# Kernel optimization log

Measured on AMD Instinct MI355X. Metric: run time of the kernel, lower is better.

The kernel has to match this reference:

```python
import jax, jax.numpy as jnp
import numpy as np

D = 256; H = 8; DH = D // H; FF = 1024; L = 2048; M = 1024


def _mlp(x, w0, b0, w1, b1, w2, b2):
    # 3-layer MLP, relu on all but last (matches MLP class)
    x = jax.nn.relu(x @ w0 + b0)
    x = jax.nn.relu(x @ w1 + b1)
    return x @ w2 + b2


def _ln(x, g, b, eps=1e-5):
    m = jnp.mean(x, axis=-1, keepdims=True)
    v = jnp.var(x, axis=-1, keepdims=True)
    return (x - m) * jax.lax.rsqrt(v + eps) * g + b


def setup_inputs():
    key = jax.random.key(0)
    ks = jax.random.split(key, 16)
    p = lambda i, shape: jax.random.normal(ks[i], shape, jnp.float32) * 0.02
    z = lambda *s: jnp.zeros(s, jnp.float32)
    o = lambda *s: jnp.ones(s, jnp.float32)
    # positions: ego covers [0, L), agent covers [L-M, 2L-M) -> exactly M shared positions
    return {
        'ego_q': jax.random.normal(ks[0], (1, L, D), jnp.float32),
        'agent_q': jax.random.normal(ks[1], (1, L, D), jnp.float32),
        'ego_pos': jnp.arange(L, dtype=jnp.int32),
        'agent_pos': jnp.arange(L, dtype=jnp.int32) + (L - M),
        'n_match': M,
        'fw0': p(2, (2 * D, D)), 'fb0': z(D),
        'fw1': p(3, (D, D)), 'fb1': z(D),
        'fw2': p(4, (D, D)), 'fb2': z(D),
        'wq': p(5, (D, D)), 'bq': z(D),
        'wk': p(6, (D, D)), 'bk': z(D),
        'wv': p(7, (D, D)), 'bv': z(D),
        'wo': p(8, (D, D)), 'bo': z(D),
        'g1': o(D), 'be1': z(D),
        'l1w': p(9, (D, FF)), 'l1b': z(FF),
        'l2w': p(10, (FF, D)), 'l2b': z(D),
        'g2': o(D), 'be2': z(D),
    }


def reference(ego_q, agent_q, ego_pos, agent_pos, n_match,
              fw0, fb0, fw1, fb1, fw2, fb2,
              wq, bq, wk, bk, wv, bv, wo, bo,
              g1, be1, l1w, l1b, l2w, l2b, g2, be2):
    La = agent_pos.shape[0]
    # vectorized replacement of the per-position dict/loop grouping:
    # for each ego position, find a matching agent position (positions sorted+unique)
    idx = jnp.clip(jnp.searchsorted(agent_pos, ego_pos), 0, La - 1)
    matched = (agent_pos[idx] == ego_pos)                     # (L,)
    pair = jnp.concatenate([ego_q, agent_q[:, idx, :]], axis=-1)  # (1, L, 2D)
    fused = _mlp(pair, fw0, fb0, fw1, fb1, fw2, fb2)          # (1, L, D)
    ego_out = jnp.where(matched[None, :, None], fused, ego_q)
    # agent queries whose positions are NOT in ego's set: indices [n_match, La)
    q = jnp.concatenate([ego_out, agent_q[:, n_match:, :]], axis=1)  # (1, 2L-M, D)
    kv = jnp.concatenate([ego_q, agent_q], axis=1)                   # (1, 2L, D)
    # MultiheadAttention (batch_first, eval mode -> no dropout)
    qh = (q @ wq + bq).reshape(1, -1, H, DH)
    kh = (kv @ wk + bk).reshape(1, -1, H, DH)
    vh = (kv @ wv + bv).reshape(1, -1, H, DH)
    scores = jnp.einsum('bqhd,bkhd->bhqk', qh, kh) * (1.0 / np.sqrt(DH))
    attn = jax.nn.softmax(scores, axis=-1)
    o = jnp.einsum('bhqk,bkhd->bqhd', attn, vh).reshape(1, -1, D) @ wo + bo
    x = _ln(q + o, g1, be1)
    ff = jax.nn.relu(x @ l1w + l1b) @ l2w + l2b
    return _ln(x + ff, g2, be2)
```

## Files before the change

kernel.cpp:

```cpp
#include <hip/hip_runtime.h>
#include <hip/hip_bf16.h>

typedef __hip_bfloat16 bf16;
typedef __bf16 bf16x8 __attribute__((ext_vector_type(8)));
typedef float  f32x16 __attribute__((ext_vector_type(16)));

__device__ __forceinline__ bool is_bf16_flag(const unsigned* g1w) {
    return *g1w == 0x3F803F80u;
}

__device__ __forceinline__ unsigned cvt_pk_bf16(float lo, float hi) {
    unsigned w;
    asm("v_cvt_pk_bf16_f32 %0, %1, %2" : "=v"(w) : "v"(lo), "v"(hi));
    return w;
}
__device__ __forceinline__ void permlane32_swap(unsigned& a, unsigned& b) {
    asm("v_permlane32_swap_b32 %0, %1" : "+v"(a), "+v"(b));
}

union FragU { unsigned u[4]; uint4 q; bf16x8 v; };

__device__ __forceinline__ float loadf(const void* p, size_t i, bool isb) {
    return isb ? __bfloat162float(((const bf16*)p)[i]) : ((const float*)p)[i];
}

__device__ __forceinline__ float4 load4rt(const void* p, size_t i, bool isb) {
    if (isb) {
        uint2 u = *(const uint2*)((const bf16*)p + i);
        float4 f;
        f.x = __uint_as_float(u.x << 16);
        f.y = __uint_as_float(u.x & 0xFFFF0000u);
        f.z = __uint_as_float(u.y << 16);
        f.w = __uint_as_float(u.y & 0xFFFF0000u);
        return f;
    }
    return *(const float4*)((const float*)p + i);
}

__device__ __forceinline__ void store4b(bf16* p, float4 v) {
    uint2 w;
    w.x = cvt_pk_bf16(v.x, v.y);
    w.y = cvt_pk_bf16(v.z, v.w);
    *(uint2*)p = w;
}

__device__ __forceinline__ float4 load4b(const bf16* p) {
    uint2 u = *(const uint2*)p;
    float4 f;
    f.x = __uint_as_float(u.x << 16);
    f.y = __uint_as_float(u.x & 0xFFFF0000u);
    f.z = __uint_as_float(u.y << 16);
    f.w = __uint_as_float(u.y & 0xFFFF0000u);
    return f;
}

__device__ __forceinline__ uint4 load8rt(const void* p, size_t off, bool isb) {
    if (isb) return *(const uint4*)((const bf16*)p + off);
    const float* f = (const float*)p + off;
    float4 a = *(const float4*)f, b = *(const float4*)(f + 4);
    uint4 r;
    r.x = cvt_pk_bf16(a.x, a.y); r.y = cvt_pk_bf16(a.z, a.w);
    r.z = cvt_pk_bf16(b.x, b.y); r.w = cvt_pk_bf16(b.z, b.w);
    return r;
}

struct RowSrc { const void* p; size_t base; bool b16; };
__device__ __forceinline__ uint4 load8src(const RowSrc& s, int c) {
    return load8rt(s.p, s.base + c, s.b16);
}

#define NCVT 13
#define NWT 9
struct PreArgs {
    const void* csrc[NCVT];
    float*      cdst[NCVT];
    float       cscale[NCVT];
    int         cn4[NCVT];
    int         cblk_end[NCVT];
    int         cvt_blocks;
    const void* wsrc[NWT];
    bf16*       wdst[NWT];
    int         wK[NWT];
    int         wN[NWT];
    float       wscale[NWT];
    int         wblk_end[NWT];
    int         wt_blocks;
    const int*  epos; const int* apos;
    int         La;
    int*        mflag;
    int*        midx;
};

__global__ void preprocess_kernel(PreArgs a, const unsigned* __restrict__ g1w) {
    bool isb = is_bf16_flag(g1w);
    __shared__ float ld[64][65];
    int b = blockIdx.x;
    int tid = threadIdx.x;
    if (b < a.cvt_blocks) {
        int t = 0;
        while (b >= a.cblk_end[t]) t++;
        int base = (t == 0) ? 0 : a.cblk_end[t - 1];
        int i = (b - base) * 256 + tid;
        if (i >= a.cn4[t]) return;
        float sc = a.cscale[t];
        float4 r = load4rt(a.csrc[t], (size_t)i * 4, isb);
        r.x *= sc; r.y *= sc; r.z *= sc; r.w *= sc;
        ((float4*)a.cdst[t])[i] = r;
    } else if (b < a.cvt_blocks + a.wt_blocks) {
        b -= a.cvt_blocks;
        int w = 0;
        while (b >= a.wblk_end[w]) w++;
        int base = (w == 0) ? 0 : a.wblk_end[w - 1];
        int tt = b - base;
        int tn = a.wN[w] >> 6;
        int kr = (tt / tn) * 64, nc = (tt % tn) * 64;
        int N = a.wN[w], K = a.wK[w];
        float sc = a.wscale[w];
        const void* src = a.wsrc[w];
#pragma unroll
        for (int i = 0; i < 16; i++) {
            int f = tid + i * 256;
            int r = f >> 6, c = f & 63;
            ld[r][c] = loadf(src, (size_t)(kr + r) * N + nc + c, isb) * sc;
        }
        __syncthreads();
        bf16* dst = a.wdst[w];
#pragma unroll
        for (int i = 0; i < 16; i++) {
            int f = tid + i * 256;
            int c = f >> 6, r = f & 63;
            dst[(size_t)(nc + c) * K + kr + r] = __float2bfloat16(ld[r][c]);
        }
    } else {
        b -= a.cvt_blocks + a.wt_blocks;
        int row = b * 256 + tid;
        int p = a.epos[row];
        int lo = 0, hi = a.La;
        while (lo < hi) { int mid = (lo + hi) >> 1; if (a.apos[mid] < p) lo = mid + 1; else hi = mid; }
        int idx = lo < a.La - 1 ? lo : a.La - 1;
        a.midx[row] = idx;
        a.mflag[row] = (a.apos[idx] == p) ? 1 : 0;
    }
}

template<int RELU, class AL>
__device__ __forceinline__ void gemm_core(AL aload, const bf16* __restrict__ Bt,
                                          const float* __restrict__ bias, bf16* __restrict__ C,
                                          int K, int ldb, int ldc,
                                          int bm, int bn, bool addBias,
                                          char* sA, char* sB) {
    const int t = threadIdx.x;
    const int lane = t & 63, wave = t >> 6;
    const int hi = lane >> 5, ql = lane & 31;
    const int wm = (wave & 1) * 32, wn = (wave >> 1) * 32;

    const int r0 = t >> 3, ch0 = t & 7;
    const int r1 = 32 + r0;
    const int wb0 = (r0 * 128 + ch0 * 16) ^ ((r0 & 7) << 4);
    const int wb1 = (r1 * 128 + ch0 * 16) ^ ((r1 & 7) << 4);

    uint4 ra0, ra1, rb0, rb1;
    ra0 = aload(0, ch0 * 8);
    ra1 = aload(1, ch0 * 8);
    rb0 = *(const uint4*)&Bt[(size_t)(bn + r0) * ldb + ch0 * 8];
    rb1 = *(const uint4*)&Bt[(size_t)(bn + r1) * ldb + ch0 * 8];

    f32x16 acc = {};
    const int swzA = ((wm + ql) & 7) << 4;
    const int swzB = ((wn + ql) & 7) << 4;
    const int rowA = (wm + ql) * 128;
    const int rowB = (wn + ql) * 128;

    for (int k0 = 0; k0 < K; k0 += 64) {
        __syncthreads();
        *(uint4*)(sA + wb0) = ra0;
        *(uint4*)(sA + wb1) = ra1;
        *(uint4*)(sB + wb0) = rb0;
        *(uint4*)(sB + wb1) = rb1;
        if (k0 + 64 < K) {
            int kn = k0 + 64;
            ra0 = aload(0, kn + ch0 * 8);
            ra1 = aload(1, kn + ch0 * 8);
            rb0 = *(const uint4*)&Bt[(size_t)(bn + r0) * ldb + kn + ch0 * 8];
            rb1 = *(const uint4*)&Bt[(size_t)(bn + r1) * ldb + kn + ch0 * 8];
        }
        __syncthreads();
#pragma unroll
        for (int kc = 0; kc < 4; kc++) {
            FragU af, bf_;
            af.q  = *(const uint4*)(sA + ((rowA + kc * 32 + hi * 16) ^ swzA));
            bf_.q = *(const uint4*)(sB + ((rowB + kc * 32 + hi * 16) ^ swzB));
            acc = __builtin_amdgcn_mfma_f32_32x32x16_bf16(af.v, bf_.v, acc, 0, 0, 0);
        }
    }

    int gn = bn + wn + ql;
    float bsv = addBias ? bias[gn] : 0.f;
#pragma unroll
    for (int r = 0; r < 16; r++) {
        int mrow = (r & 3) + 8 * (r >> 2) + 4 * hi;
        float v = acc[r] + bsv;
        if (RELU) v = fmaxf(v, 0.f);
        C[(size_t)(bm + wm + mrow) * ldc + gn] = __float2bfloat16(v);
    }
}

template<int RELU>
__launch_bounds__(256)
__global__ void gemm_bf16_kernel(const bf16* __restrict__ A, const bf16* __restrict__ Bt,
                                 const float* __restrict__ bias, bf16* __restrict__ C,
                                 int M, int N, int K, int lda, int ldb, int ldc) {
    __shared__ __align__(16) char sA[64 * 128];
    __shared__ __align__(16) char sB[64 * 128];
    const int z = blockIdx.z;
    const bf16* Az = A + (size_t)z * K;
    const int bm = blockIdx.y * 64;
    const int r0 = bm + (threadIdx.x >> 3), r1 = r0 + 32;
    auto al = [&](int i, int c) {
        return *(const uint4*)&Az[(size_t)(i ? r1 : r0) * lda + c];
    };
    gemm_core<RELU>(al, Bt + (size_t)z * K, bias, C + (size_t)z * M * ldc,
                    K, ldb, ldc, bm, blockIdx.x * 64, z == 0, sA, sB);
}

template<int RELU>
__launch_bounds__(256)
__global__ void gemm_pair_kernel(const void* __restrict__ ego, const void* __restrict__ agent,
                                 const int* __restrict__ midx,
                                 const bf16* __restrict__ Bt, const float* __restrict__ bias,
                                 bf16* __restrict__ C, int ldc,
                                 const unsigned* __restrict__ g1w) {
    __shared__ __align__(16) char sA[64 * 128];
    __shared__ __align__(16) char sB[64 * 128];
    bool isb = is_bf16_flag(g1w);
    const int bm = blockIdx.y * 64;
    const int r0 = bm + (threadIdx.x >> 3), r1 = r0 + 32;
    const int m0 = midx[r0], m1 = midx[r1];
    auto al = [&](int i, int c) {
        int r = i ? r1 : r0, m = i ? m1 : m0;
        if (c < 256) return load8rt(ego, (size_t)r * 256 + c, isb);
        return load8rt(agent, (size_t)m * 256 + (c - 256), isb);
    };
    gemm_core<RELU>(al, Bt, bias, C, 512, 512, ldc, bm, blockIdx.x * 64, true, sA, sB);
}

__device__ __forceinline__ RowSrc q_row_src(int r, const void* ego, const void* agent,
                                            const bf16* fused, const int* mflag,
                                            int L, int Mm, bool isb) {
    RowSrc s;
    if (r < L) {
        if (mflag[r]) { s.p = fused; s.base = (size_t)r * 256; s.b16 = true; }
        else          { s.p = ego;   s.base = (size_t)r * 256; s.b16 = isb; }
    } else { s.p = agent; s.base = (size_t)(Mm + r - L) * 256; s.b16 = isb; }
    return s;
}

__launch_bounds__(256)
__global__ void gemm_qkv_kernel(const void* __restrict__ ego, const void* __restrict__ agent,
                                const bf16* __restrict__ fused, const int* __restrict__ mflag,
                                int L, int Mm,
                                const bf16* __restrict__ wqt, const bf16* __restrict__ wkvt,
                                const float* __restrict__ bq, const float* __restrict__ bkv,
                                bf16* __restrict__ qh, bf16* __restrict__ kvh, int nblk0,
                                const unsigned* __restrict__ g1w) {
    __shared__ __align__(16) char sA[64 * 128];
    __shared__ __align__(16) char sB[64 * 128];
    bool isb = is_bf16_flag(g1w);
    int b = blockIdx.x;
    int rl = threadIdx.x >> 3;
    if (b < nblk0) {
        int bn = (b & 3) * 64, bm = (b >> 2) * 64;
        RowSrc s0 = q_row_src(bm + rl, ego, agent, fused, mflag, L, Mm, isb);
        RowSrc s1 = q_row_src(bm + rl + 32, ego, agent, fused, mflag, L, Mm, isb);
        auto al = [&](int i, int c) { return load8src(i ? s1 : s0, c); };
        gemm_core<0>(al, wqt, bq, qh, 256, 256, 256, bm, bn, true, sA, sB);
    } else {
        b -= nblk0;
        int bn = (b & 7) * 64, bm = (b >> 3) * 64;
        int r0 = bm + rl, r1 = r0 + 32;
        RowSrc s0, s1;
        if (r0 < L) { s0.p = ego; s0.base = (size_t)r0 * 256; }
        else        { s0.p = agent; s0.base = (size_t)(r0 - L) * 256; }
        if (r1 < L) { s1.p = ego; s1.base = (size_t)r1 * 256; }
        else        { s1.p = agent; s1.base = (size_t)(r1 - L) * 256; }
        s0.b16 = isb; s1.b16 = isb;
        auto al = [&](int i, int c) { return load8src(i ? s1 : s0, c); };
        gemm_core<0>(al, wkvt, bkv, kvh, 256, 256, 512, bm, bn, true, sA, sB);
    }
}

#define SPLITS 8

__launch_bounds__(256)
__global__ void attn_mfma_kernel(const bf16* __restrict__ qh,
                                 const bf16* __restrict__ kvh,
                                 float* __restrict__ pm, float* __restrict__ pl,
                                 bf16* __restrict__ pacc,
                                 int Nq, int Nk) {
    __shared__ __align__(16) char sK[64 * 128];
    __shared__ __align__(16) char sV[32 * 128];

    const int nx = Nq >> 7;
    int bid = blockIdx.x;
    int per = (nx * 8 * SPLITS) >> 3;
    int swz = (bid & 7) * per + (bid >> 3);
    const int x = swz % nx;
    int rem = swz / nx;
    const int h = rem & 7;
    const int z = rem >> 3;

    const int t = threadIdx.x;
    const int wave = t >> 6, lane = t & 63;
    const int ql = lane & 31, hi = lane >> 5;
    const int qbase = x * 128 + wave * 32;
    const int kbeg = z * (Nk / SPLITS);
    const int nkk = Nk / SPLITS;

    FragU qf0, qf1;
    {
        const bf16* qp = qh + (size_t)(qbase + ql) * 256 + h * 32;
        qf0.q = *(const uint4*)(qp + hi * 8);
        qf1.q = *(const uint4*)(qp + 16 + hi * 8);
    }

    float mrun = -1e30f, lrun = 0.f;
    f32x16 acc = {};

    const int skey = t >> 2, sch = t & 3;
    const int kwb = (skey * 128 + sch * 16) ^ ((skey & 7) << 4);

    uint4 rk = *(const uint4*)(kvh + (size_t)(kbeg + skey) * 512 + h * 32 + sch * 8);
    uint4 rv = *(const uint4*)(kvh + (size_t)(kbeg + lane) * 512 + 256 + h * 32 + wave * 8);

#pragma unroll 1
    for (int t0 = 0; t0 < nkk; t0 += 64) {
        __syncthreads();
        *(uint4*)(sK + kwb) = rk;
        {
            unsigned short sv[8] = {
                (unsigned short)(rv.x), (unsigned short)(rv.x >> 16),
                (unsigned short)(rv.y), (unsigned short)(rv.y >> 16),
                (unsigned short)(rv.z), (unsigned short)(rv.z >> 16),
                (unsigned short)(rv.w), (unsigned short)(rv.w >> 16)};
#pragma unroll
            for (int i = 0; i < 8; i++) {
                int dh = wave * 8 + i;
                *(unsigned short*)(sV + dh * 128 + ((lane * 2) ^ (i << 4))) = sv[i];
            }
        }
        if (t0 + 64 < nkk) {
            rk = *(const uint4*)(kvh + (size_t)(kbeg + t0 + 64 + skey) * 512 + h * 32 + sch * 8);
            rv = *(const uint4*)(kvh + (size_t)(kbeg + t0 + 64 + lane) * 512 + 256 + h * 32 + wave * 8);
        }
        __syncthreads();

        FragU ka, kb;
        f32x16 s0 = {}, s1 = {};
        {
            int row0 = ql, row1 = 32 + ql;
            int swzk = (ql & 7) << 4;
            __builtin_amdgcn_s_setprio(1);
            ka.q = *(const uint4*)(sK + ((row0 * 128 + hi * 16) ^ swzk));
            s0 = __builtin_amdgcn_mfma_f32_32x32x16_bf16(ka.v, qf0.v, s0, 0, 0, 0);
            ka.q = *(const uint4*)(sK + ((row0 * 128 + 32 + hi * 16) ^ swzk));
            s0 = __builtin_amdgcn_mfma_f32_32x32x16_bf16(ka.v, qf1.v, s0, 0, 0, 0);
            kb.q = *(const uint4*)(sK + ((row1 * 128 + hi * 16) ^ swzk));
            s1 = __builtin_amdgcn_mfma_f32_32x32x16_bf16(kb.v, qf0.v, s1, 0, 0, 0);
            kb.q = *(const uint4*)(sK + ((row1 * 128 + 32 + hi * 16) ^ swzk));
            s1 = __builtin_amdgcn_mfma_f32_32x32x16_bf16(kb.v, qf1.v, s1, 0, 0, 0);
            __builtin_amdgcn_s_setprio(0);
        }

        float tm = -1e30f;
#pragma unroll
        for (int r = 0; r < 16; r++) tm = fmaxf(tm, fmaxf(s0[r], s1[r]));
        tm = fmaxf(tm, __shfl_xor(tm, 32));
        if (!__all(tm <= mrun)) {
            float mn = fmaxf(mrun, tm);
            float cf = __builtin_amdgcn_exp2f(mrun - mn);
            mrun = mn;
#pragma unroll
            for (int r = 0; r < 16; r++) acc[r] *= cf;
            lrun *= cf;
        }

        float p0[16], p1[16];
        float ls = 0.f;
#pragma unroll
        for (int r = 0; r < 16; r++) { p0[r] = __builtin_amdgcn_exp2f(s0[r] - mrun); ls += p0[r]; }
#pragma unroll
        for (int r = 0; r < 16; r++) { p1[r] = __builtin_amdgcn_exp2f(s1[r] - mrun); ls += p1[r]; }
        ls += __shfl_xor(ls, 32);
        lrun += ls;

        int swzk = (ql & 7) << 4;
        FragU vf, pa;
        __builtin_amdgcn_s_setprio(1);
        {
            unsigned a = cvt_pk_bf16(p0[0], p0[1]),  b = cvt_pk_bf16(p0[2], p0[3]);
            unsigned c = cvt_pk_bf16(p0[4], p0[5]),  d = cvt_pk_bf16(p0[6], p0[7]);
            permlane32_swap(a, c); permlane32_swap(b, d);
            pa.u[0] = a; pa.u[1] = b; pa.u[2] = c; pa.u[3] = d;
            vf.q = *(const uint4*)(sV + ((ql * 128 + hi * 16) ^ swzk));
            acc = __builtin_amdgcn_mfma_f32_32x32x16_bf16(vf.v, pa.v, acc, 0, 0, 0);
            unsigned e = cvt_pk_bf16(p0[8], p0[9]),   f = cvt_pk_bf16(p0[10], p0[11]);
            unsigned g = cvt_pk_bf16(p0[12], p0[13]), h2 = cvt_pk_bf16(p0[14], p0[15]);
            permlane32_swap(e, g); permlane32_swap(f, h2);
            pa.u[0] = e; pa.u[1] = f; pa.u[2] = g; pa.u[3] = h2;
            vf.q = *(const uint4*)(sV + ((ql * 128 + 32 + hi * 16) ^ swzk));
            acc = __builtin_amdgcn_mfma_f32_32x32x16_bf16(vf.v, pa.v, acc, 0, 0, 0);
        }
        {
            unsigned a = cvt_pk_bf16(p1[0], p1[1]),  b = cvt_pk_bf16(p1[2], p1[3]);
            unsigned c = cvt_pk_bf16(p1[4], p1[5]),  d = cvt_pk_bf16(p1[6], p1[7]);
            permlane32_swap(a, c); permlane32_swap(b, d);
            pa.u[0] = a; pa.u[1] = b; pa.u[2] = c; pa.u[3] = d;
            vf.q = *(const uint4*)(sV + ((ql * 128 + 64 + hi * 16) ^ swzk));
            acc = __builtin_amdgcn_mfma_f32_32x32x16_bf16(vf.v, pa.v, acc, 0, 0, 0);
            unsigned e = cvt_pk_bf16(p1[8], p1[9]),   f = cvt_pk_bf16(p1[10], p1[11]);
            unsigned g = cvt_pk_bf16(p1[12], p1[13]), h2 = cvt_pk_bf16(p1[14], p1[15]);
            permlane32_swap(e, g); permlane32_swap(f, h2);
            pa.u[0] = e; pa.u[1] = f; pa.u[2] = g; pa.u[3] = h2;
            vf.q = *(const uint4*)(sV + ((ql * 128 + 96 + hi * 16) ^ swzk));
            acc = __builtin_amdgcn_mfma_f32_32x32x16_bf16(vf.v, pa.v, acc, 0, 0, 0);
        }
        __builtin_amdgcn_s_setprio(0);
    }

    if (hi == 0) {
        pm[((size_t)z * 8 + h) * Nq + qbase + ql] = mrun;
        pl[((size_t)z * 8 + h) * Nq + qbase + ql] = lrun;
    }
#pragma unroll
    for (int r = 0; r < 16; r++) {
        int dh = (r & 3) + 8 * (r >> 2) + 4 * hi;
        pacc[(((size_t)z * 8 + h) * 32 + dh) * (size_t)Nq + qbase + ql] = __float2bfloat16(acc[r]);
    }
}

__global__ void attn_merge_kernel(const float* __restrict__ pm, const float* __restrict__ pl,
                                  const bf16* __restrict__ pacc, bf16* __restrict__ o, int Nq) {
    int q = blockIdx.x * 256 + threadIdx.x;
    int h = blockIdx.y, dg = blockIdx.z;
    float ml[SPLITS];
    float M = -1e30f;
#pragma unroll
    for (int s = 0; s < SPLITS; s++) {
        ml[s] = pm[((size_t)s * 8 + h) * Nq + q];
        M = fmaxf(M, ml[s]);
    }
    float L = 0.f;
    float w[SPLITS];
#pragma unroll
    for (int s = 0; s < SPLITS; s++) {
        w[s] = __builtin_amdgcn_exp2f(ml[s] - M);
        L += pl[((size_t)s * 8 + h) * Nq + q] * w[s];
    }
    float inv = 1.f / L;
#pragma unroll
    for (int j = 0; j < 4; j++) {
        int d = dg * 4 + j;
        float a = 0.f;
#pragma unroll
        for (int s = 0; s < SPLITS; s++)
            a += __bfloat162float(pacc[(((size_t)s * 8 + h) * 32 + d) * (size_t)Nq + q]) * w[s];
        o[(size_t)q * 256 + h * 32 + d] = __float2bfloat16(a * inv);
    }
}

template<int GATHER>
__global__ void ln_kernel(const bf16* __restrict__ a, const bf16* __restrict__ b,
                          const bf16* __restrict__ c,
                          const float* __restrict__ g, const float* __restrict__ be,
                          bf16* __restrict__ outf16, void* __restrict__ outb,
                          const void* __restrict__ ego, const void* __restrict__ agent,
                          const bf16* __restrict__ fused, const int* __restrict__ mflag,
                          int L, int Mm,
                          const unsigned* __restrict__ g1w) {
    bool isb = is_bf16_flag(g1w);
    int wave = threadIdx.x >> 6, lane = threadIdx.x & 63;
    int row = blockIdx.x * 4 + wave;
    int col = lane * 4;
    size_t base = (size_t)row * 256 + col;
    float4 av;
    if (GATHER) {
        if (row < L) av = mflag[row] ? load4b(fused + base)
                                     : load4rt(ego, base, isb);
        else av = load4rt(agent, (size_t)(Mm + row - L) * 256 + col, isb);
    } else {
        av = load4b(a + base);
    }
    float4 bv = load4b(b + base);
    float x0 = av.x + bv.x, x1 = av.y + bv.y, x2 = av.z + bv.z, x3 = av.w + bv.w;
    if (c) {
        float4 cv = load4b(c + base);
        x0 += cv.x; x1 += cv.y; x2 += cv.z; x3 += cv.w;
    }
    float s  = x0 + x1 + x2 + x3;
    float s2 = x0 * x0 + x1 * x1 + x2 * x2 + x3 * x3;
#pragma unroll
    for (int off = 32; off; off >>= 1) { s += __shfl_xor(s, off); s2 += __shfl_xor(s2, off); }
    float mean = s * (1.f / 256.f);
    float var  = s2 * (1.f / 256.f) - mean * mean;
    float rs = rsqrtf(var + 1e-5f);
    float4 gv = *(const float4*)(g + col);
    float4 bev = *(const float4*)(be + col);
    float y0 = (x0 - mean) * rs * gv.x + bev.x;
    float y1 = (x1 - mean) * rs * gv.y + bev.y;
    float y2 = (x2 - mean) * rs * gv.z + bev.z;
    float y3 = (x3 - mean) * rs * gv.w + bev.w;
    if (outf16) {
        store4b(outf16 + base, make_float4(y0, y1, y2, y3));
    } else if (is_bf16_flag(g1w)) {
        store4b((bf16*)outb + base, make_float4(y0, y1, y2, y3));
    } else {
        *(float4*)((float*)outb + base) = make_float4(y0, y1, y2, y3);
    }
}

extern "C" void kernel_launch(void* const* d_in, const int* in_sizes, int n_in,
                              void* d_out, int out_size, void* d_ws, size_t ws_size,
                              hipStream_t stream) {
    const int Dd = 256;
    const int L  = in_sizes[2];
    const int La = in_sizes[3];
    const int Nk = L + La;
    const int Nq = out_size / Dd;
    const int Mm = L + La - Nq;
    const float scale = 0.17677669529663687f * 1.4426950408889634f;

    const unsigned* g1w = (const unsigned*)d_in[19];

    float* W = (float*)d_ws;
    size_t off = 0;
    auto alloc = [&](size_t n) { size_t o = off; off += n; return o; };
    (void)ws_size; (void)n_in;

    size_t o_fb0 = alloc(256), o_fb1 = alloc(256), o_fb2 = alloc(256);
    size_t o_bq = alloc(256), o_bkv = alloc(512), o_bo = alloc(256);
    size_t o_g1 = alloc(256), o_be1 = alloc(256);
    size_t o_l1b = alloc(1024), o_l2b = alloc(256);
    size_t o_g2 = alloc(256), o_be2 = alloc(256);

    size_t o_fw0t = alloc(65536), o_fw1t = alloc(32768), o_fw2t = alloc(32768);
    size_t o_wqt = alloc(32768), o_wkvt = alloc(65536), o_wot = alloc(32768);
    size_t o_l1wt = alloc(131072), o_l2wt = alloc(131072);
    size_t o_h1 = alloc((size_t)L * 128), o_h2 = alloc((size_t)L * 128);
    size_t o_fused = alloc((size_t)L * 128);
    size_t o_qh  = alloc((size_t)Nq * 128);
    size_t o_kvh = alloc((size_t)Nk * 256);
    size_t o_ao  = alloc((size_t)Nq * 128);
    size_t o_opp = alloc((size_t)Nq * 256);
    size_t o_x   = alloc((size_t)Nq * 128);
    size_t o_ff1 = alloc((size_t)Nq * 512);
    size_t o_ff2p = alloc((size_t)Nq * 256);
    size_t o_pacc = alloc((size_t)SPLITS * 8 * 16 * Nq);
    size_t o_pm   = alloc((size_t)SPLITS * 8 * Nq);
    size_t o_pl   = alloc((size_t)SPLITS * 8 * Nq);
    size_t o_ints = alloc((size_t)2 * L);
    int* mflag = (int*)(W + o_ints);
    int* midx  = mflag + L;

    auto B16 = [&](size_t o) { return (bf16*)(W + o); };

    {
        PreArgs pa;
        const int csrcs[NCVT] = {6, 8, 10, 12, 14, 16, 18, 19, 20, 22, 24, 25, 26};
        const size_t cdsts[NCVT] = {o_fb0, o_fb1, o_fb2, o_bq, o_bkv, o_bkv + 256, o_bo,
                                    o_g1, o_be1, o_l1b, o_l2b, o_g2, o_be2};
        int blk = 0;
        for (int i = 0; i < NCVT; i++) {
            pa.csrc[i] = d_in[csrcs[i]];
            pa.cdst[i] = W + cdsts[i];
            pa.cscale[i] = (csrcs[i] == 12) ? scale : 1.0f;
            pa.cn4[i] = in_sizes[csrcs[i]] / 4;
            blk += (pa.cn4[i] + 255) / 256;
            pa.cblk_end[i] = blk;
        }
        pa.cvt_blocks = blk;

        const int wsrcs[NWT] = {5, 7, 9, 11, 13, 15, 17, 21, 23};
        bf16* wdsts[NWT] = {B16(o_fw0t), B16(o_fw1t), B16(o_fw2t), B16(o_wqt),
                            B16(o_wkvt), B16(o_wkvt) + 65536, B16(o_wot),
                            B16(o_l1wt), B16(o_l2wt)};
        const int Ks[NWT] = {512, 256, 256, 256, 256, 256, 256, 256, 1024};
        const int Ns[NWT] = {256, 256, 256, 256, 256, 256, 256, 1024, 256};
        int wblk = 0;
        for (int i = 0; i < NWT; i++) {
            pa.wsrc[i] = d_in[wsrcs[i]];
            pa.wdst[i] = wdsts[i];
            pa.wK[i] = Ks[i]; pa.wN[i] = Ns[i];
            pa.wscale[i] = (wsrcs[i] == 11) ? scale : 1.0f;
            wblk += (Ks[i] / 64) * (Ns[i] / 64);
            pa.wblk_end[i] = wblk;
        }
        pa.wt_blocks = wblk;

        pa.epos = (const int*)d_in[2]; pa.apos = (const int*)d_in[3];
        pa.La = La; pa.mflag = mflag; pa.midx = midx;

        int total = pa.cvt_blocks + pa.wt_blocks + L / 256;
        preprocess_kernel<<<total, 256, 0, stream>>>(pa, g1w);
    }

    gemm_pair_kernel<1><<<dim3(4, L/64), 256, 0, stream>>>(d_in[0], d_in[1], midx,
                                                           B16(o_fw0t), W + o_fb0, B16(o_h1), 256, g1w);
    gemm_bf16_kernel<1><<<dim3(4, L/64), 256, 0, stream>>>(B16(o_h1), B16(o_fw1t), W + o_fb1, B16(o_h2),    L, 256, 256, 256, 256, 256);
    gemm_bf16_kernel<0><<<dim3(4, L/64), 256, 0, stream>>>(B16(o_h2), B16(o_fw2t), W + o_fb2, B16(o_fused), L, 256, 256, 256, 256, 256);

    {
        int nblk0 = 4 * (Nq / 64);
        int nblk1 = 8 * (Nk / 64);
        gemm_qkv_kernel<<<nblk0 + nblk1, 256, 0, stream>>>(d_in[0], d_in[1], B16(o_fused), mflag,
                                                           L, Mm, B16(o_wqt), B16(o_wkvt),
                                                           W + o_bq, W + o_bkv,
                                                           B16(o_qh), B16(o_kvh), nblk0, g1w);
    }

    attn_mfma_kernel<<<(Nq/128) * 8 * SPLITS, 256, 0, stream>>>(B16(o_qh), B16(o_kvh),
                                                                W + o_pm, W + o_pl, B16(o_pacc),
                                                                Nq, Nk);
    attn_merge_kernel<<<dim3(Nq/256, 8, 8), 256, 0, stream>>>(W + o_pm, W + o_pl, B16(o_pacc),
                                                              B16(o_ao), Nq);

    gemm_bf16_kernel<0><<<dim3(4, Nq/64, 2), 256, 0, stream>>>(B16(o_ao), B16(o_wot), W + o_bo, B16(o_opp), Nq, 256, 128, 256, 256, 256);
    ln_kernel<1><<<Nq / 4, 256, 0, stream>>>(nullptr, B16(o_opp), B16(o_opp) + (size_t)Nq * 256,
                                             W + o_g1, W + o_be1, B16(o_x), nullptr,
                                             d_in[0], d_in[1], B16(o_fused), mflag, L, Mm, g1w);

    gemm_bf16_kernel<1><<<dim3(16, Nq/64), 256, 0, stream>>>(B16(o_x),   B16(o_l1wt), W + o_l1b, B16(o_ff1), Nq, 1024, 256, 256, 256, 1024);
    gemm_bf16_kernel<0><<<dim3(4,  Nq/64, 2), 256, 0, stream>>>(B16(o_ff1), B16(o_l2wt), W + o_l2b, B16(o_ff2p), Nq, 256, 512, 1024, 1024, 256);
    ln_kernel<0><<<Nq / 4, 256, 0, stream>>>(B16(o_x), B16(o_ff2p), B16(o_ff2p) + (size_t)Nq * 256,
                                             W + o_g2, W + o_be2, nullptr, d_out,
                                             nullptr, nullptr, nullptr, nullptr, L, Mm, g1w);
}
```

Measured before the change: 100.2 us.

## Fuse the three-layer pair MLP into one kernel and double-buffer attention LDS

The three separate GEMM launches for the pair MLP become one kernel. Each block computes all three layers for a 64-row band and keeps the hidden activations in LDS bands, so the h1/h2 global buffers and two launches go away. The cost is that only L/64 blocks run, each working through twelve output tiles in sequence with no load prefetch and a large LDS footprint, so parallelism drops sharply. Separately, the attention kernel now double-buffers its K/V LDS tiles to remove one barrier per iteration, and the s_setprio hints are dropped.

```diff
diff --git a/kernel.cpp b/kernel.cpp
--- a/kernel.cpp
+++ b/kernel.cpp
@@ -223,25 +223,115 @@
                     K, ldb, ldc, bm, blockIdx.x * 64, z == 0, sA, sB);
 }
 
-template<int RELU>
 __launch_bounds__(256)
-__global__ void gemm_pair_kernel(const void* __restrict__ ego, const void* __restrict__ agent,
+__global__ void mlp_fused_kernel(const void* __restrict__ ego, const void* __restrict__ agent,
                                  const int* __restrict__ midx,
-                                 const bf16* __restrict__ Bt, const float* __restrict__ bias,
-                                 bf16* __restrict__ C, int ldc,
+                                 const bf16* __restrict__ w1t, const float* __restrict__ b1,
+                                 const bf16* __restrict__ w2t, const float* __restrict__ b2,
+                                 const bf16* __restrict__ w3t, const float* __restrict__ b3,
+                                 bf16* __restrict__ fusedOut,
                                  const unsigned* __restrict__ g1w) {
+    __shared__ __align__(16) char band1[64 * 512];
+    __shared__ __align__(16) char band2[64 * 512];
     __shared__ __align__(16) char sA[64 * 128];
     __shared__ __align__(16) char sB[64 * 128];
     bool isb = is_bf16_flag(g1w);
-    const int bm = blockIdx.y * 64;
-    const int r0 = bm + (threadIdx.x >> 3), r1 = r0 + 32;
-    const int m0 = midx[r0], m1 = midx[r1];
-    auto al = [&](int i, int c) {
-        int r = i ? r1 : r0, m = i ? m1 : m0;
-        if (c < 256) return load8rt(ego, (size_t)r * 256 + c, isb);
-        return load8rt(agent, (size_t)m * 256 + (c - 256), isb);
-    };
-    gemm_core<RELU>(al, Bt, bias, C, 512, 512, ldc, bm, blockIdx.x * 64, true, sA, sB);
+    const int t = threadIdx.x;
+    const int lane = t & 63, wave = t >> 6;
+    const int hi = lane >> 5, ql = lane & 31;
+    const int wm = (wave & 1) * 32, wn = (wave >> 1) * 32;
+    const int bm = blockIdx.x * 64;
+    const int r0 = t >> 3, ch0 = t & 7;
+    const int gr0 = bm + r0, gr1 = gr0 + 32;
+    const int m0 = midx[gr0], m1 = midx[gr1];
+    const int wb0 = (r0 * 128 + ch0 * 16) ^ ((r0 & 7) << 4);
+    const int wb1 = ((32 + r0) * 128 + ch0 * 16) ^ (((32 + r0) & 7) << 4);
+    const int rowA = wm + ql;
+    const int swzA = (rowA & 7) << 4;
+    const int swzB = ((wn + ql) & 7) << 4;
+    const int rowBo = (wn + ql) * 128;
+    const int rowAo = rowA * 128;
+
+    for (int bn = 0; bn < 256; bn += 64) {
+        f32x16 acc = {};
+        for (int k0 = 0; k0 < 512; k0 += 64) {
+            __syncthreads();
+            int c = k0 + ch0 * 8;
+            uint4 ra0 = (c < 256) ? load8rt(ego, (size_t)gr0 * 256 + c, isb)
+                                  : load8rt(agent, (size_t)m0 * 256 + (c - 256), isb);
+            uint4 ra1 = (c < 256) ? load8rt(ego, (size_t)gr1 * 256 + c, isb)
+                                  : load8rt(agent, (size_t)m1 * 256 + (c - 256), isb);
+            *(uint4*)(sA + wb0) = ra0;
+            *(uint4*)(sA + wb1) = ra1;
+            *(uint4*)(sB + wb0) = *(const uint4*)&w1t[(size_t)(bn + r0) * 512 + c];
+            *(uint4*)(sB + wb1) = *(const uint4*)&w1t[(size_t)(bn + 32 + r0) * 512 + c];
+            __syncthreads();
+#pragma unroll
+            for (int kc = 0; kc < 4; kc++) {
+                FragU af, bf_;
+                af.q  = *(const uint4*)(sA + ((rowAo + kc * 32 + hi * 16) ^ swzA));
+                bf_.q = *(const uint4*)(sB + ((rowBo + kc * 32 + hi * 16) ^ swzB));
+                acc = __builtin_amdgcn_mfma_f32_32x32x16_bf16(af.v, bf_.v, acc, 0, 0, 0);
+            }
+        }
+        int gn = bn + wn + ql;
+        float bsv = b1[gn];
+#pragma unroll
+        for (int r = 0; r < 16; r++) {
+            int br = wm + ((r & 3) + 8 * (r >> 2) + 4 * hi);
+            float v = fmaxf(acc[r] + bsv, 0.f);
+            *(bf16*)(band1 + br * 512 + ((gn * 2) ^ ((br & 7) << 4))) = __float2bfloat16(v);
+        }
+    }
+    for (int bn = 0; bn < 256; bn += 64) {
+        f32x16 acc = {};
+        for (int k0 = 0; k0 < 256; k0 += 64) {
+            __syncthreads();
+            int c = k0 + ch0 * 8;
+            *(uint4*)(sB + wb0) = *(const uint4*)&w2t[(size_t)(bn + r0) * 256 + c];
+            *(uint4*)(sB + wb1) = *(const uint4*)&w2t[(size_t)(bn + 32 + r0) * 256 + c];
+            __syncthreads();
+#pragma unroll
+            for (int kc = 0; kc < 4; kc++) {
+                FragU af, bf_;
+                af.q  = *(const uint4*)(band1 + rowA * 512 + ((k0 * 2 + kc * 32 + hi * 16) ^ swzA));
+                bf_.q = *(const uint4*)(sB + ((rowBo + kc * 32 + hi * 16) ^ swzB));
+                acc = __builtin_amdgcn_mfma_f32_32x32x16_bf16(af.v, bf_.v, acc, 0, 0, 0);
+            }
+        }
+        int gn = bn + wn + ql;
+        float bsv = b2[gn];
+#pragma unroll
+        for (int r = 0; r < 16; r++) {
+            int br = wm + ((r & 3) + 8 * (r >> 2) + 4 * hi);
+            float v = fmaxf(acc[r] + bsv, 0.f);
+            *(bf16*)(band2 + br * 512 + ((gn * 2) ^ ((br & 7) << 4))) = __float2bfloat16(v);
+        }
+    }
+    for (int bn = 0; bn < 256; bn += 64) {
+        f32x16 acc = {};
+        for (int k0 = 0; k0 < 256; k0 += 64) {
+            __syncthreads();
+            int c = k0 + ch0 * 8;
+            *(uint4*)(sB + wb0) = *(const uint4*)&w3t[(size_t)(bn + r0) * 256 + c];
+            *(uint4*)(sB + wb1) = *(const uint4*)&w3t[(size_t)(bn + 32 + r0) * 256 + c];
+            __syncthreads();
+#pragma unroll
+            for (int kc = 0; kc < 4; kc++) {
+                FragU af, bf_;
+                af.q  = *(const uint4*)(band2 + rowA * 512 + ((k0 * 2 + kc * 32 + hi * 16) ^ swzA));
+                bf_.q = *(const uint4*)(sB + ((rowBo + kc * 32 + hi * 16) ^ swzB));
+                acc = __builtin_amdgcn_mfma_f32_32x32x16_bf16(af.v, bf_.v, acc, 0, 0, 0);
+            }
+        }
+        int gn = bn + wn + ql;
+        float bsv = b3[gn];
+#pragma unroll
+        for (int r = 0; r < 16; r++) {
+            int mrow = (r & 3) + 8 * (r >> 2) + 4 * hi;
+            fusedOut[(size_t)(bm + wm + mrow) * 256 + gn] = __float2bfloat16(acc[r] + bsv);
+        }
+    }
 }
 
 __device__ __forceinline__ RowSrc q_row_src(int r, const void* ego, const void* agent,
@@ -297,8 +387,8 @@
                                  float* __restrict__ pm, float* __restrict__ pl,
                                  bf16* __restrict__ pacc,
                                  int Nq, int Nk) {
-    __shared__ __align__(16) char sK[64 * 128];
-    __shared__ __align__(16) char sV[32 * 128];
+    __shared__ __align__(16) char sK[2][64 * 128];
+    __shared__ __align__(16) char sV[2][32 * 128];
 
     const int nx = Nq >> 7;
     int bid = blockIdx.x;
@@ -332,10 +422,12 @@
     uint4 rk = *(const uint4*)(kvh + (size_t)(kbeg + skey) * 512 + h * 32 + sch * 8);
     uint4 rv = *(const uint4*)(kvh + (size_t)(kbeg + lane) * 512 + 256 + h * 32 + wave * 8);
 
+    int cur = 0;
 #pragma unroll 1
     for (int t0 = 0; t0 < nkk; t0 += 64) {
-        __syncthreads();
-        *(uint4*)(sK + kwb) = rk;
+        char* sKc = sK[cur];
+        char* sVc = sV[cur];
+        *(uint4*)(sKc + kwb) = rk;
         {
             unsigned short sv[8] = {
                 (unsigned short)(rv.x), (unsigned short)(rv.x >> 16),
@@ -345,7 +437,7 @@
 #pragma unroll
             for (int i = 0; i < 8; i++) {
                 int dh = wave * 8 + i;
-                *(unsigned short*)(sV + dh * 128 + ((lane * 2) ^ (i << 4))) = sv[i];
+                *(unsigned short*)(sVc + dh * 128 + ((lane * 2) ^ (i << 4))) = sv[i];
             }
         }
         if (t0 + 64 < nkk) {
@@ -359,16 +451,14 @@
         {
             int row0 = ql, row1 = 32 + ql;
             int swzk = (ql & 7) << 4;
-            __builtin_amdgcn_s_setprio(1);
-            ka.q = *(const uint4*)(sK + ((row0 * 128 + hi * 16) ^ swzk));
+            ka.q = *(const uint4*)(sKc + ((row0 * 128 + hi * 16) ^ swzk));
             s0 = __builtin_amdgcn_mfma_f32_32x32x16_bf16(ka.v, qf0.v, s0, 0, 0, 0);
-            ka.q = *(const uint4*)(sK + ((row0 * 128 + 32 + hi * 16) ^ swzk));
+            ka.q = *(const uint4*)(sKc + ((row0 * 128 + 32 + hi * 16) ^ swzk));
             s0 = __builtin_amdgcn_mfma_f32_32x32x16_bf16(ka.v, qf1.v, s0, 0, 0, 0);
-            kb.q = *(const uint4*)(sK + ((row1 * 128 + hi * 16) ^ swzk));
+            kb.q = *(const uint4*)(sKc + ((row1 * 128 + hi * 16) ^ swzk));
             s1 = __builtin_amdgcn_mfma_f32_32x32x16_bf16(kb.v, qf0.v, s1, 0, 0, 0);
-            kb.q = *(const uint4*)(sK + ((row1 * 128 + 32 + hi * 16) ^ swzk));
+            kb.q = *(const uint4*)(sKc + ((row1 * 128 + 32 + hi * 16) ^ swzk));
             s1 = __builtin_amdgcn_mfma_f32_32x32x16_bf16(kb.v, qf1.v, s1, 0, 0, 0);
-            __builtin_amdgcn_s_setprio(0);
         }
 
         float tm = -1e30f;
@@ -395,19 +485,18 @@
 
         int swzk = (ql & 7) << 4;
         FragU vf, pa;
-        __builtin_amdgcn_s_setprio(1);
         {
             unsigned a = cvt_pk_bf16(p0[0], p0[1]),  b = cvt_pk_bf16(p0[2], p0[3]);
             unsigned c = cvt_pk_bf16(p0[4], p0[5]),  d = cvt_pk_bf16(p0[6], p0[7]);
             permlane32_swap(a, c); permlane32_swap(b, d);
             pa.u[0] = a; pa.u[1] = b; pa.u[2] = c; pa.u[3] = d;
-            vf.q = *(const uint4*)(sV + ((ql * 128 + hi * 16) ^ swzk));
+            vf.q = *(const uint4*)(sVc + ((ql * 128 + hi * 16) ^ swzk));
             acc = __builtin_amdgcn_mfma_f32_32x32x16_bf16(vf.v, pa.v, acc, 0, 0, 0);
             unsigned e = cvt_pk_bf16(p0[8], p0[9]),   f = cvt_pk_bf16(p0[10], p0[11]);
             unsigned g = cvt_pk_bf16(p0[12], p0[13]), h2 = cvt_pk_bf16(p0[14], p0[15]);
             permlane32_swap(e, g); permlane32_swap(f, h2);
             pa.u[0] = e; pa.u[1] = f; pa.u[2] = g; pa.u[3] = h2;
-            vf.q = *(const uint4*)(sV + ((ql * 128 + 32 + hi * 16) ^ swzk));
+            vf.q = *(const uint4*)(sVc + ((ql * 128 + 32 + hi * 16) ^ swzk));
             acc = __builtin_amdgcn_mfma_f32_32x32x16_bf16(vf.v, pa.v, acc, 0, 0, 0);
         }
         {
@@ -415,16 +504,16 @@
             unsigned c = cvt_pk_bf16(p1[4], p1[5]),  d = cvt_pk_bf16(p1[6], p1[7]);
             permlane32_swap(a, c); permlane32_swap(b, d);
             pa.u[0] = a; pa.u[1] = b; pa.u[2] = c; pa.u[3] = d;
-            vf.q = *(const uint4*)(sV + ((ql * 128 + 64 + hi * 16) ^ swzk));
+            vf.q = *(const uint4*)(sVc + ((ql * 128 + 64 + hi * 16) ^ swzk));
             acc = __builtin_amdgcn_mfma_f32_32x32x16_bf16(vf.v, pa.v, acc, 0, 0, 0);
             unsigned e = cvt_pk_bf16(p1[8], p1[9]),   f = cvt_pk_bf16(p1[10], p1[11]);
             unsigned g = cvt_pk_bf16(p1[12], p1[13]), h2 = cvt_pk_bf16(p1[14], p1[15]);
             permlane32_swap(e, g); permlane32_swap(f, h2);
             pa.u[0] = e; pa.u[1] = f; pa.u[2] = g; pa.u[3] = h2;
-            vf.q = *(const uint4*)(sV + ((ql * 128 + 96 + hi * 16) ^ swzk));
+            vf.q = *(const uint4*)(sVc + ((ql * 128 + 96 + hi * 16) ^ swzk));
             acc = __builtin_amdgcn_mfma_f32_32x32x16_bf16(vf.v, pa.v, acc, 0, 0, 0);
         }
-        __builtin_amdgcn_s_setprio(0);
+        cur ^= 1;
     }
 
     if (hi == 0) {
@@ -545,7 +634,6 @@
     size_t o_fw0t = alloc(65536), o_fw1t = alloc(32768), o_fw2t = alloc(32768);
     size_t o_wqt = alloc(32768), o_wkvt = alloc(65536), o_wot = alloc(32768);
     size_t o_l1wt = alloc(131072), o_l2wt = alloc(131072);
-    size_t o_h1 = alloc((size_t)L * 128), o_h2 = alloc((size_t)L * 128);
     size_t o_fused = alloc((size_t)L * 128);
     size_t o_qh  = alloc((size_t)Nq * 128);
     size_t o_kvh = alloc((size_t)Nk * 256);
@@ -603,10 +691,11 @@
         preprocess_kernel<<<total, 256, 0, stream>>>(pa, g1w);
     }
 
-    gemm_pair_kernel<1><<<dim3(4, L/64), 256, 0, stream>>>(d_in[0], d_in[1], midx,
-                                                           B16(o_fw0t), W + o_fb0, B16(o_h1), 256, g1w);
-    gemm_bf16_kernel<1><<<dim3(4, L/64), 256, 0, stream>>>(B16(o_h1), B16(o_fw1t), W + o_fb1, B16(o_h2),    L, 256, 256, 256, 256, 256);
-    gemm_bf16_kernel<0><<<dim3(4, L/64), 256, 0, stream>>>(B16(o_h2), B16(o_fw2t), W + o_fb2, B16(o_fused), L, 256, 256, 256, 256, 256);
+    mlp_fused_kernel<<<L / 64, 256, 0, stream>>>(d_in[0], d_in[1], midx,
+                                                 B16(o_fw0t), W + o_fb0,
+                                                 B16(o_fw1t), W + o_fb1,
+                                                 B16(o_fw2t), W + o_fb2,
+                                                 B16(o_fused), g1w);
 
     {
         int nblk0 = 4 * (Nq / 64);
```

After: 132.6 us. 1.32x slower.
